# Kernel optimization log

Hardware: AMD Instinct MI355X
Metric: run time of the kernel (lower is better)

Reference implementation:

```python
import jax, jax.numpy as jnp
import numpy as np

HIDDEN = 768
MLP = 4 * HIDDEN

def layernorm(x, g, b, eps=1e-5):
    mu = jnp.mean(x, axis=-1, keepdims=True)
    var = jnp.var(x, axis=-1, keepdims=True)
    return (x - mu) * jax.lax.rsqrt(var + eps) * g + b

def setup_inputs() -> dict:
    key = jax.random.key(0)
    ks = jax.random.split(key, 10)
    b, l, h = 8, 1024, HIDDEN
    s = 1.0 / np.sqrt(h)
    inp = {
        "x": jax.random.normal(ks[0], (b, l, h), dtype=jnp.float32),
        "Wq": jax.random.normal(ks[1], (h, h), dtype=jnp.float32) * s,
        "Wk": jax.random.normal(ks[2], (h, h), dtype=jnp.float32) * s,
        "Wv": jax.random.normal(ks[3], (h, h), dtype=jnp.float32) * s,
        "Wo": jax.random.normal(ks[4], (h, h), dtype=jnp.float32) * s,
        "W1": jax.random.normal(ks[5], (h, MLP), dtype=jnp.float32) * s,
        "b1": jnp.zeros((MLP,), dtype=jnp.float32),
        "W2": jax.random.normal(ks[6], (MLP, h), dtype=jnp.float32) * (1.0 / np.sqrt(MLP)),
        "b2": jnp.zeros((h,), dtype=jnp.float32),
        "g1": jnp.ones((h,), dtype=jnp.float32),
        "be1": jnp.zeros((h,), dtype=jnp.float32),
        "g2": jnp.ones((h,), dtype=jnp.float32),
        "be2": jnp.zeros((h,), dtype=jnp.float32),
        "n_heads": 12,
    }
    return inp

def reference(x, Wq, Wk, Wv, Wo, W1, b1, W2, b2, g1, be1, g2, be2, n_heads):
    b, l, h = x.shape
    d = h // n_heads
    # NOTE: faithful to source — heads are the LAST axis of a plain reshape,
    # and the second einsum contracts with K (not V), reproducing the original code.
    q = (x @ Wq).reshape(b, l, d, n_heads)
    k = (x @ Wk).reshape(b, l, d, n_heads)
    v = (x @ Wv).reshape(b, l, d, n_heads)  # computed but unused downstream, as in source
    scores = jnp.einsum('bldn,bmdn->blmn', q, k) / (d ** 0.5)
    attn = jax.nn.softmax(scores, axis=2)  # softmax over m (dim=2), as in source
    ctx = jnp.einsum('blmn,bmdn->bldn', attn, k).reshape(b, l, h)
    attn_out = ctx @ Wo
    x = x + attn_out
    x = layernorm(x, g1, be1)
    ff = (jax.nn.gelu(x @ W1 + b1, approximate=False) @ W2) + b2
    x = x + ff
    x = layernorm(x, g2, be2)
    return x
```

## Files before the change

kernel.cpp:

```cpp
#include <hip/hip_runtime.h>
#include <math.h>

typedef unsigned short u16;
typedef unsigned int u32;
typedef short bf16x8 __attribute__((ext_vector_type(8)));
typedef float f32x4 __attribute__((ext_vector_type(4)));

#define MFMA(a, b, c) __builtin_amdgcn_mfma_f32_16x16x32_bf16((a), (b), (c), 0, 0, 0)

#define GLOAD_LDS16(g, l)                                                              \
    __builtin_amdgcn_global_load_lds((const __attribute__((address_space(1))) void*)(g), \
                                     (__attribute__((address_space(3))) void*)(l), 16, 0, 0)

__device__ __forceinline__ u16 f2bf(float f) {
    u32 u = __float_as_uint(f);
    u32 r = (u + 0x7fffu + ((u >> 16) & 1u)) >> 16;
    return (u16)r;
}

__device__ __forceinline__ float fast_gelu(float z) {
    float u = fminf(1.5957691216f * z * (1.0f + 0.044715f * z * z), 80.0f);
    float e = __expf(u);
    float r = __builtin_amdgcn_rcpf(e + 1.0f);
    return z * e * r;
}

__global__ __launch_bounds__(256) void f32_to_bf16_k(const float* __restrict__ in,
                                                     u16* __restrict__ out) {
    size_t i = ((size_t)blockIdx.x * 256 + threadIdx.x) * 8;
    const float4* p = reinterpret_cast<const float4*>(in + i);
    float4 a = p[0], b = p[1];
    union { u16 u[8]; uint4 v; } o;
    o.u[0] = f2bf(a.x); o.u[1] = f2bf(a.y); o.u[2] = f2bf(a.z); o.u[3] = f2bf(a.w);
    o.u[4] = f2bf(b.x); o.u[5] = f2bf(b.y); o.u[6] = f2bf(b.z); o.u[7] = f2bf(b.w);
    *reinterpret_cast<uint4*>(out + i) = o.v;
}

__global__ __launch_bounds__(256) void transpose_bf16_k(const float* __restrict__ in,
                                                        u16* __restrict__ out,
                                                        int K, int N) {
    __shared__ float tile[64][65];
    int k0 = blockIdx.y * 64, n0 = blockIdx.x * 64;
    int t = threadIdx.x;
    for (int p = 0; p < 16; p++) {
        int idx = t + p * 256;
        int r = idx >> 6, c = idx & 63;
        tile[r][c] = in[(size_t)(k0 + r) * N + n0 + c];
    }
    __syncthreads();
    for (int p = 0; p < 16; p++) {
        int idx = t + p * 256;
        int nr = idx >> 6, nc = idx & 63;
        out[(size_t)(n0 + nr) * K + k0 + nc] = f2bf(tile[nc][nr]);
    }
}

__global__ __launch_bounds__(256) void transpose_wo_k(const float* __restrict__ in,
                                                      u16* __restrict__ out) {
    __shared__ float tile[96][65];
    int k0 = blockIdx.y * 96, n0 = blockIdx.x * 64;
    int t = threadIdx.x;
    for (int p = 0; p < 24; p++) {
        int idx = t + p * 256;
        int r = idx >> 6, c = idx & 63;
        tile[r][c] = in[(size_t)(k0 + r) * 768 + n0 + c];
    }
    __syncthreads();
    for (int p = 0; p < 3; p++) {
        int idx = t + p * 256;
        int c = idx / 12, n = idx % 12;
        union { u16 u[8]; uint4 v; } o;
        for (int j = 0; j < 8; j++) o.u[j] = f2bf(tile[j * 12 + n][c]);
        *reinterpret_cast<uint4*>(&out[(size_t)(n0 + c) * 768 + n * 64 + blockIdx.y * 8]) = o.v;
    }
}

__global__ __launch_bounds__(256) void head_pack_k(const u16* __restrict__ in, int ld,
                                                   u16* __restrict__ out) {
    __shared__ u16 tile[16 * 768];
    int b = blockIdx.y;
    int l0 = blockIdx.x * 16;
    int t = threadIdx.x;
    for (int p = 0; p < 6; p++) {
        int c = t + p * 256;
        int li = c / 96, dc = c % 96;
        *reinterpret_cast<uint4*>(&tile[li * 768 + dc * 8]) =
            *reinterpret_cast<const uint4*>(&in[(size_t)(b * 1024 + l0 + li) * ld + dc * 8]);
    }
    __syncthreads();
    for (int p = 0; p < 6; p++) {
        int c = t + p * 256;
        int n = c >> 7, rem = c & 127, li = rem >> 3, k8 = rem & 7;
        union { u16 u[8]; uint4 v; } o;
        for (int j = 0; j < 8; j++) o.u[j] = tile[li * 768 + (k8 * 8 + j) * 12 + n];
        *reinterpret_cast<uint4*>(&out[(size_t)((b * 12 + n) * 1024 + l0 + li) * 64 + k8 * 8]) = o.v;
    }
}

template <int EPI, int TM, bool AH = false>
__global__ __launch_bounds__(256) void gemm_bt_k(const u16* __restrict__ A,
                                                 const u16* __restrict__ BT,
                                                 int M, int N, int K,
                                                 float* __restrict__ outF,
                                                 u16* __restrict__ outB,
                                                 const float* __restrict__ resid,
                                                 const float* __restrict__ bias) {
    constexpr int MI = TM / 32;
    __shared__ __align__(16) u16 As[3][TM * 32];
    __shared__ __align__(16) u16 Bs[3][128 * 32];
    int m0 = blockIdx.y * TM, n0 = blockIdx.x * 128;
    int t = threadIdx.x;
    int wave = t >> 6, lane = t & 63;
    int wr = (wave >> 1) * (TM / 2), wc = (wave & 1) * 64;
    int ln = lane & 15, quad = lane >> 4;
    int sw = quad ^ ((ln >> 1) & 3);

    int e0 = t, e1 = t + 256;
    int r0 = e0 >> 2, c0 = (e0 & 3) ^ ((r0 >> 1) & 3);
    int r1 = e1 >> 2, c1 = (e1 & 3) ^ ((r1 >> 1) & 3);
    const u16* A0 = A + (size_t)(m0 + r0) * K + c0 * 8;
    const u16* A1 = A + (size_t)(m0 + r1) * K + c1 * 8;
    const u16* B0 = BT + (size_t)(n0 + r0) * K + c0 * 8;
    const u16* B1 = BT + (size_t)(n0 + r1) * K + c1 * 8;
    const u16* Abase = nullptr;
    if constexpr (AH) {
        int m = m0 + r0;
        Abase = A + ((size_t)(m >> 10) * 12288 + (m & 1023)) * 64;
    }

    int nk = K >> 5;

    f32x4 acc[MI][4];
    for (int i = 0; i < MI; i++)
        for (int j = 0; j < 4; j++)
            for (int r = 0; r < 4; r++) acc[i][j][r] = 0.0f;

    for (int s = 0; s < 2; s++) {
        if constexpr (AH) {
            int col8 = s * 4 + c0;
            GLOAD_LDS16(Abase + (col8 >> 3) * 65536 + (col8 & 7) * 8, &As[s][e0 * 8]);
        } else {
            GLOAD_LDS16(A0 + s * 32, &As[s][e0 * 8]);
            if constexpr (TM == 128) GLOAD_LDS16(A1 + s * 32, &As[s][e1 * 8]);
        }
        GLOAD_LDS16(B0 + s * 32, &Bs[s][e0 * 8]);
        GLOAD_LDS16(B1 + s * 32, &Bs[s][e1 * 8]);
    }

    for (int k = 0; k < nk; k++) {
        if constexpr (TM == 64) asm volatile("s_waitcnt vmcnt(3)" ::: "memory");
        else                    asm volatile("s_waitcnt vmcnt(4)" ::: "memory");
        asm volatile("s_barrier" ::: "memory");
        {
            int ks = k + 2 < nk ? k + 2 : nk - 1;
            int bi = (k + 2) % 3;
            if constexpr (AH) {
                int col8 = ks * 4 + c0;
                GLOAD_LDS16(Abase + (col8 >> 3) * 65536 + (col8 & 7) * 8, &As[bi][e0 * 8]);
            } else {
                GLOAD_LDS16(A0 + ks * 32, &As[bi][e0 * 8]);
                if constexpr (TM == 128) GLOAD_LDS16(A1 + ks * 32, &As[bi][e1 * 8]);
            }
            GLOAD_LDS16(B0 + ks * 32, &Bs[bi][e0 * 8]);
            GLOAD_LDS16(B1 + ks * 32, &Bs[bi][e1 * 8]);
        }
        const u16* as = As[k % 3];
        const u16* bs = Bs[k % 3];
        bf16x8 afr[MI], bfr[4];
        for (int i = 0; i < MI; i++)
            afr[i] = *reinterpret_cast<const bf16x8*>(&as[(wr + i * 16 + ln) * 32 + sw * 8]);
        for (int j = 0; j < 4; j++)
            bfr[j] = *reinterpret_cast<const bf16x8*>(&bs[(wc + j * 16 + ln) * 32 + sw * 8]);
        for (int i = 0; i < MI; i++)
            for (int j = 0; j < 4; j++)
                acc[i][j] = MFMA(afr[i], bfr[j], acc[i][j]);
    }

    for (int i = 0; i < MI; i++) {
        for (int j = 0; j < 4; j++) {
            int col = n0 + wc + j * 16 + ln;
            for (int r = 0; r < 4; r++) {
                int row = m0 + wr + i * 16 + quad * 4 + r;
                size_t idx = (size_t)row * N + col;
                float v = acc[i][j][r];
                if constexpr (EPI == 0) {
                    outB[idx] = f2bf(v);
                } else if constexpr (EPI == 1) {
                    outF[idx] = resid[idx] + v;
                } else if constexpr (EPI == 2) {
                    outB[idx] = f2bf(fast_gelu(v + bias[col]));
                } else if constexpr (EPI == 3) {
                    outF[idx] = resid[idx] + v + bias[col];
                } else {
                    outB[idx] = f2bf(col < 768 ? v * 0.125f : v);
                }
            }
        }
    }
}

__global__ __launch_bounds__(256) void attention_k(const u16* __restrict__ QB, int ldq,
                                                   const u16* __restrict__ KH,
                                                   u16* __restrict__ CTXH) {
    __shared__ __align__(16) u16 Ks[64 * 72];
    __shared__ __align__(16) u16 KsT[64 * 72];
    __shared__ __align__(16) u16 Pl[4][16 * 64];
    int bh = blockIdx.y;
    int b = bh / 12, n = bh % 12;
    int l0 = blockIdx.x * 64;
    int t = threadIdx.x, wave = t >> 6, lane = t & 63;
    int ln = lane & 15, quad = lane >> 4;
    int lw = l0 + wave * 16;

    bf16x8 a0, a1;
    {
        union { u16 u[8]; bf16x8 v; } q0, q1;
        const u16* qrow = QB + (size_t)(b * 1024 + lw + ln) * ldq + n;
        for (int j = 0; j < 8; j++) {
            q0.u[j] = qrow[(quad * 8 + j) * 12];
            q1.u[j] = qrow[(32 + quad * 8 + j) * 12];
        }
        a0 = q0.v; a1 = q1.v;
    }

    f32x4 o[4];
    for (int dt = 0; dt < 4; dt++)
        for (int r = 0; r < 4; r++) o[dt][r] = 0.0f;
    float lst[4];
    for (int r = 0; r < 4; r++) lst[r] = 0.0f;

    const u16* Kbase = KH + (size_t)bh * 1024 * 64;
    int mi = t & 63, ds = (t >> 6) * 16;
    int psw = (ln >> 2) & 3;

    union { u16 u[8]; uint4 v; } kva, kvb;
    kva.v = *reinterpret_cast<const uint4*>(&Kbase[(size_t)mi * 64 + ds]);
    kvb.v = *reinterpret_cast<const uint4*>(&Kbase[(size_t)mi * 64 + ds + 8]);

    for (int mb = 0; mb < 16; mb++) {
        __syncthreads();
        *reinterpret_cast<uint4*>(&Ks[mi * 72 + ds]) = kva.v;
        *reinterpret_cast<uint4*>(&Ks[mi * 72 + ds + 8]) = kvb.v;
        for (int j = 0; j < 8; j++) KsT[(ds + j) * 72 + mi] = kva.u[j];
        for (int j = 0; j < 8; j++) KsT[(ds + 8 + j) * 72 + mi] = kvb.u[j];
        __syncthreads();

        {
            int mnext = (mb + 1 < 16 ? mb + 1 : 15) * 64;
            kva.v = *reinterpret_cast<const uint4*>(&Kbase[(size_t)(mnext + mi) * 64 + ds]);
            kvb.v = *reinterpret_cast<const uint4*>(&Kbase[(size_t)(mnext + mi) * 64 + ds + 8]);
        }

        f32x4 st[4];
        for (int nt = 0; nt < 4; nt++) {
            bf16x8 bk0 = *reinterpret_cast<bf16x8*>(&Ks[(nt * 16 + ln) * 72 + quad * 8]);
            bf16x8 bk1 = *reinterpret_cast<bf16x8*>(&Ks[(nt * 16 + ln) * 72 + 32 + quad * 8]);
            f32x4 z;
            for (int r = 0; r < 4; r++) z[r] = 0.0f;
            z = MFMA(a0, bk0, z);
            st[nt] = MFMA(a1, bk1, z);
        }

        for (int r = 0; r < 4; r++) {
            int row = quad * 4 + r;
            float psum = 0.0f;
            for (int nt = 0; nt < 4; nt++) {
                float p = __expf(fminf(st[nt][r], 30.0f));
                psum += p;
                Pl[wave][row * 64 + (((nt * 2 + (ln >> 3)) ^ quad) * 8) + (ln & 7)] = f2bf(p);
            }
            lst[r] += psum;
        }

        bf16x8 pf0 = *reinterpret_cast<bf16x8*>(&Pl[wave][ln * 64 + (quad ^ psw) * 8]);
        bf16x8 pf1 = *reinterpret_cast<bf16x8*>(&Pl[wave][ln * 64 + (quad ^ psw) * 8 + 32]);
        for (int dt = 0; dt < 4; dt++) {
            bf16x8 bk0 = *reinterpret_cast<bf16x8*>(&KsT[(dt * 16 + ln) * 72 + quad * 8]);
            bf16x8 bk1 = *reinterpret_cast<bf16x8*>(&KsT[(dt * 16 + ln) * 72 + 32 + quad * 8]);
            o[dt] = MFMA(pf0, bk0, o[dt]);
            o[dt] = MFMA(pf1, bk1, o[dt]);
        }
    }

    for (int r = 0; r < 4; r++)
        for (int off = 1; off < 16; off <<= 1) lst[r] += __shfl_xor(lst[r], off, 64);

    u16* out = CTXH + (size_t)bh * 1024 * 64;
    for (int r = 0; r < 4; r++) {
        float inv = 1.0f / lst[r];
        int row = lw + quad * 4 + r;
        for (int dt = 0; dt < 4; dt++)
            out[(size_t)row * 64 + dt * 16 + ln] = f2bf(o[dt][r] * inv);
    }
}

__global__ __launch_bounds__(256) void layernorm_k(const float* __restrict__ in,
                                                   float* __restrict__ outF,
                                                   u16* __restrict__ outB,
                                                   const float* __restrict__ g,
                                                   const float* __restrict__ be) {
    __shared__ float red[8];
    int row = blockIdx.x;
    int t = threadIdx.x;
    const float* p = in + (size_t)row * 768;
    float v0 = p[t], v1 = p[t + 256], v2 = p[t + 512];
    float s = v0 + v1 + v2;
    float ss = v0 * v0 + v1 * v1 + v2 * v2;
    for (int off = 32; off >= 1; off >>= 1) {
        s += __shfl_xor(s, off, 64);
        ss += __shfl_xor(ss, off, 64);
    }
    int wave = t >> 6, lane = t & 63;
    if (lane == 0) { red[wave] = s; red[4 + wave] = ss; }
    __syncthreads();
    float S = red[0] + red[1] + red[2] + red[3];
    float SS = red[4] + red[5] + red[6] + red[7];
    float mean = S * (1.0f / 768.0f);
    float var = SS * (1.0f / 768.0f) - mean * mean;
    float rstd = rsqrtf(var + 1e-5f);
    float o0 = (v0 - mean) * rstd * g[t] + be[t];
    float o1 = (v1 - mean) * rstd * g[t + 256] + be[t + 256];
    float o2 = (v2 - mean) * rstd * g[t + 512] + be[t + 512];
    float* q = outF + (size_t)row * 768;
    q[t] = o0; q[t + 256] = o1; q[t + 512] = o2;
    if (outB) {
        u16* qb = outB + (size_t)row * 768;
        qb[t] = f2bf(o0); qb[t + 256] = f2bf(o1); qb[t + 512] = f2bf(o2);
    }
}

extern "C" void kernel_launch(void* const* d_in, const int* in_sizes, int n_in,
                              void* d_out, int out_size, void* d_ws, size_t ws_size,
                              hipStream_t stream) {
    const float* x   = (const float*)d_in[0];
    const float* Wq  = (const float*)d_in[1];
    const float* Wk  = (const float*)d_in[2];
    const float* Wo  = (const float*)d_in[4];
    const float* W1  = (const float*)d_in[5];
    const float* b1  = (const float*)d_in[6];
    const float* W2  = (const float*)d_in[7];
    const float* b2  = (const float*)d_in[8];
    const float* g1  = (const float*)d_in[9];
    const float* be1 = (const float*)d_in[10];
    const float* g2  = (const float*)d_in[11];
    const float* be2 = (const float*)d_in[12];
    float* out = (float*)d_out;

    const int S = 8192, H = 768, MLP4 = 3072, H2 = 1536;

    char* ws = (char*)d_ws;
    u16* XB   = (u16*)ws;  ws += (size_t)S * H * 2;
    u16* WQKT = (u16*)ws;  ws += (size_t)H2 * H * 2;
    u16* WOT  = (u16*)ws;  ws += (size_t)H * H * 2;
    u16* W1T  = (u16*)ws;  ws += (size_t)H * MLP4 * 2;
    u16* W2T  = (u16*)ws;  ws += (size_t)H * MLP4 * 2;
    u16* QKB  = (u16*)ws;  ws += (size_t)S * H2 * 2;
    u16* KH   = (u16*)ws;  ws += (size_t)S * H * 2;
    float* Y  = (float*)ws; ws += (size_t)S * H * 4;
    u16* HB   = (u16*)ws;  ws += (size_t)S * MLP4 * 2;

    u16* CTXH = XB;
    u16* X1B  = QKB;

    f32_to_bf16_k<<<(S * H) / 2048, 256, 0, stream>>>(x, XB);
    transpose_bf16_k<<<dim3(12, 12), 256, 0, stream>>>(Wq, WQKT, H, H);
    transpose_bf16_k<<<dim3(12, 12), 256, 0, stream>>>(Wk, WQKT + (size_t)H * H, H, H);
    transpose_wo_k<<<dim3(12, 8), 256, 0, stream>>>(Wo, WOT);
    transpose_bf16_k<<<dim3(48, 12), 256, 0, stream>>>(W1, W1T, H, MLP4);
    transpose_bf16_k<<<dim3(12, 48), 256, 0, stream>>>(W2, W2T, MLP4, H);

    gemm_bt_k<4, 128><<<dim3(12, 64), 256, 0, stream>>>(XB, WQKT, S, H2, H, nullptr, QKB, nullptr, nullptr);

    head_pack_k<<<dim3(64, 8), 256, 0, stream>>>(QKB + H, H2, KH);
    attention_k<<<dim3(16, 96), 256, 0, stream>>>(QKB, H2, KH, CTXH);

    gemm_bt_k<1, 64, true><<<dim3(6, 128), 256, 0, stream>>>(CTXH, WOT, S, H, H, Y, nullptr, x, nullptr);
    layernorm_k<<<S, 256, 0, stream>>>(Y, Y, X1B, g1, be1);

    gemm_bt_k<2, 128><<<dim3(24, 64), 256, 0, stream>>>(X1B, W1T, S, MLP4, H, nullptr, HB, nullptr, b1);
    gemm_bt_k<3, 64><<<dim3(6, 128), 256, 0, stream>>>(HB, W2T, S, H, MLP4, Y, nullptr, Y, b2);
    layernorm_k<<<S, 256, 0, stream>>>(Y, out, nullptr, g2, be2);
}
```

Measured before the change: 431.3 us.

## Swizzle GEMM block order into row groups and deepen TM=64 pipeline

Replaces the 2D grid with a 1D launch and remaps block indices so groups of 8 consecutive M-tiles sweep across N together, so blocks running at the same time share A and B tiles in L2. For the TM=64 GEMM variants, the LDS pipeline goes from 3 to 4 stages, with the vmcnt wait adjusted, to hide more global load latency. The extra stage uses more shared memory per block, which may reduce occupancy.

```diff
diff --git a/kernel.cpp b/kernel.cpp
--- a/kernel.cpp
+++ b/kernel.cpp
@@ -100,15 +100,21 @@
 template <int EPI, int TM, bool AH = false>
 __global__ __launch_bounds__(256) void gemm_bt_k(const u16* __restrict__ A,
                                                  const u16* __restrict__ BT,
-                                                 int M, int N, int K,
+                                                 int M, int N, int K, int NBX,
                                                  float* __restrict__ outF,
                                                  u16* __restrict__ outB,
                                                  const float* __restrict__ resid,
                                                  const float* __restrict__ bias) {
     constexpr int MI = TM / 32;
-    __shared__ __align__(16) u16 As[3][TM * 32];
-    __shared__ __align__(16) u16 Bs[3][128 * 32];
-    int m0 = blockIdx.y * TM, n0 = blockIdx.x * 128;
+    constexpr int NS = (TM == 64) ? 4 : 3;
+    __shared__ __align__(16) u16 As[NS][TM * 32];
+    __shared__ __align__(16) u16 Bs[NS][128 * 32];
+
+    int L = blockIdx.x;
+    int bx = (L >> 3) % NBX;
+    int by = (L / (8 * NBX)) * 8 + (L & 7);
+    int m0 = by * TM, n0 = bx * 128;
+
     int t = threadIdx.x;
     int wave = t >> 6, lane = t & 63;
     int wr = (wave >> 1) * (TM / 2), wc = (wave & 1) * 64;
@@ -135,7 +141,7 @@
         for (int j = 0; j < 4; j++)
             for (int r = 0; r < 4; r++) acc[i][j][r] = 0.0f;
 
-    for (int s = 0; s < 2; s++) {
+    for (int s = 0; s < NS - 1; s++) {
         if constexpr (AH) {
             int col8 = s * 4 + c0;
             GLOAD_LDS16(Abase + (col8 >> 3) * 65536 + (col8 & 7) * 8, &As[s][e0 * 8]);
@@ -148,12 +154,12 @@
     }
 
     for (int k = 0; k < nk; k++) {
-        if constexpr (TM == 64) asm volatile("s_waitcnt vmcnt(3)" ::: "memory");
+        if constexpr (TM == 64) asm volatile("s_waitcnt vmcnt(6)" ::: "memory");
         else                    asm volatile("s_waitcnt vmcnt(4)" ::: "memory");
         asm volatile("s_barrier" ::: "memory");
         {
-            int ks = k + 2 < nk ? k + 2 : nk - 1;
-            int bi = (k + 2) % 3;
+            int ks = k + NS - 1 < nk ? k + NS - 1 : nk - 1;
+            int bi = (k + NS - 1) % NS;
             if constexpr (AH) {
                 int col8 = ks * 4 + c0;
                 GLOAD_LDS16(Abase + (col8 >> 3) * 65536 + (col8 & 7) * 8, &As[bi][e0 * 8]);
@@ -164,8 +170,8 @@
             GLOAD_LDS16(B0 + ks * 32, &Bs[bi][e0 * 8]);
             GLOAD_LDS16(B1 + ks * 32, &Bs[bi][e1 * 8]);
         }
-        const u16* as = As[k % 3];
-        const u16* bs = Bs[k % 3];
+        const u16* as = As[k % NS];
+        const u16* bs = Bs[k % NS];
         bf16x8 afr[MI], bfr[4];
         for (int i = 0; i < MI; i++)
             afr[i] = *reinterpret_cast<const bf16x8*>(&as[(wr + i * 16 + ln) * 32 + sw * 8]);
@@ -369,15 +375,15 @@
     transpose_bf16_k<<<dim3(48, 12), 256, 0, stream>>>(W1, W1T, H, MLP4);
     transpose_bf16_k<<<dim3(12, 48), 256, 0, stream>>>(W2, W2T, MLP4, H);
 
-    gemm_bt_k<4, 128><<<dim3(12, 64), 256, 0, stream>>>(XB, WQKT, S, H2, H, nullptr, QKB, nullptr, nullptr);
+    gemm_bt_k<4, 128><<<12 * 64, 256, 0, stream>>>(XB, WQKT, S, H2, H, 12, nullptr, QKB, nullptr, nullptr);
 
     head_pack_k<<<dim3(64, 8), 256, 0, stream>>>(QKB + H, H2, KH);
     attention_k<<<dim3(16, 96), 256, 0, stream>>>(QKB, H2, KH, CTXH);
 
-    gemm_bt_k<1, 64, true><<<dim3(6, 128), 256, 0, stream>>>(CTXH, WOT, S, H, H, Y, nullptr, x, nullptr);
+    gemm_bt_k<1, 64, true><<<6 * 128, 256, 0, stream>>>(CTXH, WOT, S, H, H, 6, Y, nullptr, x, nullptr);
     layernorm_k<<<S, 256, 0, stream>>>(Y, Y, X1B, g1, be1);
 
-    gemm_bt_k<2, 128><<<dim3(24, 64), 256, 0, stream>>>(X1B, W1T, S, MLP4, H, nullptr, HB, nullptr, b1);
-    gemm_bt_k<3, 64><<<dim3(6, 128), 256, 0, stream>>>(HB, W2T, S, H, MLP4, Y, nullptr, Y, b2);
+    gemm_bt_k<2, 128><<<24 * 64, 256, 0, stream>>>(X1B, W1T, S, MLP4, H, 24, nullptr, HB, nullptr, b1);
+    gemm_bt_k<3, 64><<<6 * 128, 256, 0, stream>>>(HB, W2T, S, H, MLP4, 6, Y, nullptr, Y, b2);
     layernorm_k<<<S, 256, 0, stream>>>(Y, out, nullptr, g2, be2);
 }
```

New measurement: 412.4 us. -4.4%, faster.
